# Kernel optimization log

Hardware: AMD Instinct MI355X
Metric: run time of the kernel (lower is better)

The kernel has to match this reference:

```python
import jax, jax.numpy as jnp
import numpy as np

B, ENV = 128, 512
D_IN, D1, D2 = 67, 64, 128


def _mlp(x, W1, b1, W2, b2):
    # 'deep' projection: two-layer MLP used for Q/K/V
    return jax.nn.relu(x @ W1 + b1) @ W2 + b2


def _attention(x, y, qp, kp, vp):
    # attention_mech_deep: deep Q from x, deep K/V from y, softmax over env
    Q = _mlp(x, *qp)  # (B, env, d_out)
    K = _mlp(y, *kp)
    V = _mlp(y, *vp)
    scale = 1.0 / np.sqrt(Q.shape[-1]).astype(np.float32)
    s = jnp.einsum('bid,bjd->bij', Q, K) * scale  # (B, env, env)
    return jnp.einsum('bij,bjd->bid', jax.nn.softmax(s, axis=-1), V)


def _layernorm(x, g, b, eps=1e-5):
    m = jnp.mean(x, axis=-1, keepdims=True)
    v = jnp.var(x, axis=-1, keepdims=True)
    return (x - m) * jax.lax.rsqrt(v + eps) * g + b


def _aggregate(x, W1, b1, ws, W2, b2):
    # deep_aggregator: per-node MLP + learned softmax-pooled global context
    h = jax.nn.relu(x @ W1 + b1)                      # (B, env, hid)
    alpha = jax.nn.softmax(jnp.einsum('bed,d->be', h, ws), axis=-1)
    pooled = jnp.einsum('be,bed->bd', alpha, h)[:, None, :]  # (B, 1, hid)
    return (h + pooled) @ W2 + b2                     # (B, env, out)


def setup_inputs() -> dict:
    key = jax.random.key(0)
    ks = iter(jax.random.split(key, 32))
    def p(shape, s=0.02):
        return jax.random.normal(next(ks), shape, jnp.float32) * s
    inp = {"input_graph_enc": jax.random.normal(next(ks), (B, ENV, D_IN), jnp.float32)}
    for name, di, do in [("a1", D_IN, D1), ("a2", D1, D2)]:
        for t in "qkv":
            inp[f"{name}_W{t}1"] = p((di, do))
            inp[f"{name}_b{t}1"] = jnp.zeros((do,), jnp.float32)
            inp[f"{name}_W{t}2"] = p((do, do))
            inp[f"{name}_b{t}2"] = jnp.zeros((do,), jnp.float32)
    inp["g1"] = jnp.ones((D1,), jnp.float32); inp["beta1"] = jnp.zeros((D1,), jnp.float32)
    inp["g2"] = jnp.ones((D2,), jnp.float32); inp["beta2"] = jnp.zeros((D2,), jnp.float32)
    inp["ag_W1"] = p((D2, D2)); inp["ag_b1"] = jnp.zeros((D2,), jnp.float32)
    inp["ag_ws"] = p((D2,))
    inp["ag_W2"] = p((D2, D2)); inp["ag_b2"] = jnp.zeros((D2,), jnp.float32)
    return inp


def reference(input_graph_enc,
              a1_Wq1, a1_bq1, a1_Wq2, a1_bq2,
              a1_Wk1, a1_bk1, a1_Wk2, a1_bk2,
              a1_Wv1, a1_bv1, a1_Wv2, a1_bv2,
              a2_Wq1, a2_bq1, a2_Wq2, a2_bq2,
              a2_Wk1, a2_bk1, a2_Wk2, a2_bk2,
              a2_Wv1, a2_bv1, a2_Wv2, a2_bv2,
              g1, beta1, g2, beta2,
              ag_W1, ag_b1, ag_ws, ag_W2, ag_b2):
    X = _attention(input_graph_enc, input_graph_enc,
                   (a1_Wq1, a1_bq1, a1_Wq2, a1_bq2),
                   (a1_Wk1, a1_bk1, a1_Wk2, a1_bk2),
                   (a1_Wv1, a1_bv1, a1_Wv2, a1_bv2))
    X = _layernorm(X, g1, beta1)
    X = _attention(X, X,
                   (a2_Wq1, a2_bq1, a2_Wq2, a2_bq2),
                   (a2_Wk1, a2_bk1, a2_Wk2, a2_bk2),
                   (a2_Wv1, a2_bv1, a2_Wv2, a2_bv2))
    X = _layernorm(X, g2, beta2)
    return _aggregate(X, ag_W1, ag_b1, ag_ws, ag_W2, ag_b2)  # (B, env, 128)
```

## Files before the change

### kernel.cpp

```cpp
#include <hip/hip_runtime.h>
#include <math.h>

#define ENV 512
#define NB 128

typedef __attribute__((ext_vector_type(8))) short bf16x8;
typedef __attribute__((ext_vector_type(4))) float f32x4;

__device__ inline float rsum16(float v) {
#pragma unroll
    for (int o = 8; o; o >>= 1) v += __shfl_xor(v, o, 16);
    return v;
}
__device__ inline ushort f2bf(float f) {
    unsigned u = __float_as_uint(f);
    u = u + 0x7fffu + ((u >> 16) & 1u);
    return (ushort)(u >> 16);
}
__device__ inline float bf2f(ushort h) {
    return __uint_as_float(((unsigned)h) << 16);
}

__global__ __launch_bounds__(256) void prep_kernel(
    const float* s0, const float* s1, const float* s2, const float* s3,
    const float* s4, const float* s5, const float* s6, const float* s7,
    const float* s8, const float* s9, const float* s10, const float* s11,
    const float* s12, const float* s13, ushort* wb)
{
    const float* srcs[14] = {s0,s1,s2,s3,s4,s5,s6,s7,s8,s9,s10,s11,s12,s13};
    const int Ks[14]  = {67,64,67,64,67,64, 64,128,64,128,64,128, 128,128};
    const int Cs[14]  = {64,64,64,64,64,64, 128,128,128,128,128,128, 128,128};
    const int KPs[14] = {96,64,96,64,96,64, 64,128,64,128,64,128, 128,128};
    const int offs[14]= {0,12288,20480,32768,40960,53248,
                         61440,77824,110592,126976,159744,176128,
                         208896,225280};
    const int dual[14]= {1,1,1,1,1,1,1,1,1,1,1,1,0,0};
    const int j = blockIdx.x;
    const float* src = srcs[j];
    const int K = Ks[j], C = Cs[j], KP = KPs[j], n = C * KP, d = dual[j];
    ushort* dst = wb + offs[j];
    for (int i = threadIdx.x; i < n; i += 256) {
        int c = i / KP, k = i - c * KP;
        float v = (k < K) ? src[k * C + c] : 0.f;
        ushort h = f2bf(v);
        dst[i] = h;
        if (d) dst[n + i] = f2bf(v - bf2f(h));
    }
}

__global__ __launch_bounds__(256) void xprep_kernel(
    const float* __restrict__ X, ushort* __restrict__ Xh, ushort* __restrict__ Xl)
{
    const int total = 65536 * 96;
    for (int i = blockIdx.x * 256 + threadIdx.x; i < total; i += gridDim.x * 256) {
        int r = i / 96, k = i - r * 96;
        float v = (k < 67) ? X[(long)r * 67 + k] : 0.f;
        ushort h = f2bf(v);
        Xh[i] = h;
        Xl[i] = f2bf(v - bf2f(h));
    }
}

template <int DKP, int DH, int DOUT>
__global__ __launch_bounds__(512, 1) void qk_kernel(
    const ushort* __restrict__ Xg,
    const ushort* __restrict__ Wq1, const float* __restrict__ bq1,
    const ushort* __restrict__ Wq2, const float* __restrict__ bq2,
    const ushort* __restrict__ Wk1, const float* __restrict__ bk1,
    const ushort* __restrict__ Wk2, const float* __restrict__ bk2,
    ushort* __restrict__ Qo, ushort* __restrict__ Ko)
{
    constexpr int KT1 = DKP / 32, CT1 = DH / 16, KT2 = DH / 32, CT2 = DOUT / 16;
    constexpr int W1P = DKP + 8, W2P = DH + 8, HP = DH + 8;
    __shared__ __align__(16) ushort W1s[2][DH * W1P];
    __shared__ __align__(16) ushort W2s[2][DOUT * W2P];
    __shared__ __align__(16) ushort Hs[8][16 * HP];
    const int tid = threadIdx.x, wv = tid >> 6, lid = tid & 63, g = lid >> 4, ln = lid & 15;

    for (int i = tid; i < DH * DKP / 8; i += 512) {
        int c = i / (DKP / 8), j = i - c * (DKP / 8);
        *(uint4*)&W1s[0][c * W1P + j * 8] = *(const uint4*)&Wq1[c * DKP + j * 8];
        *(uint4*)&W1s[1][c * W1P + j * 8] = *(const uint4*)&Wk1[c * DKP + j * 8];
    }
    for (int i = tid; i < DOUT * DH / 8; i += 512) {
        int c = i / (DH / 8), j = i - c * (DH / 8);
        *(uint4*)&W2s[0][c * W2P + j * 8] = *(const uint4*)&Wq2[c * DH + j * 8];
        *(uint4*)&W2s[1][c * W2P + j * 8] = *(const uint4*)&Wk2[c * DH + j * 8];
    }
    __syncthreads();

    const long row0 = (long)blockIdx.x * 128 + wv * 16;
    bf16x8 xa[KT1];
#pragma unroll
    for (int kk = 0; kk < KT1; ++kk)
        xa[kk] = *(const bf16x8*)&Xg[(row0 + ln) * DKP + kk * 32 + 8 * g];

#pragma unroll
    for (int p = 0; p < 2; ++p) {
        const ushort* w1 = W1s[p];
        const ushort* w2 = W2s[p];
        const float* b1 = p ? bk1 : bq1;
        const float* b2 = p ? bk2 : bq2;
        ushort* out = p ? Ko : Qo;
#pragma unroll
        for (int ct = 0; ct < CT1; ++ct) {
            f32x4 a = {0.f, 0.f, 0.f, 0.f};
#pragma unroll
            for (int kk = 0; kk < KT1; ++kk) {
                bf16x8 b = *(const bf16x8*)&w1[(ct * 16 + ln) * W1P + kk * 32 + 8 * g];
                a = __builtin_amdgcn_mfma_f32_16x16x32_bf16(xa[kk], b, a, 0, 0, 0);
            }
            float bb = b1[ct * 16 + ln];
#pragma unroll
            for (int i = 0; i < 4; i++)
                Hs[wv][(4 * g + i) * HP + ct * 16 + ln] = f2bf(fmaxf(a[i] + bb, 0.f));
        }
        bf16x8 ha[KT2];
#pragma unroll
        for (int kk = 0; kk < KT2; ++kk)
            ha[kk] = *(const bf16x8*)&Hs[wv][ln * HP + kk * 32 + 8 * g];
#pragma unroll
        for (int ct = 0; ct < CT2; ++ct) {
            f32x4 a = {0.f, 0.f, 0.f, 0.f};
#pragma unroll
            for (int kk = 0; kk < KT2; ++kk) {
                bf16x8 b = *(const bf16x8*)&w2[(ct * 16 + ln) * W2P + kk * 32 + 8 * g];
                a = __builtin_amdgcn_mfma_f32_16x16x32_bf16(ha[kk], b, a, 0, 0, 0);
            }
            float bb = b2[ct * 16 + ln];
            ushort* op = out + (row0 + 4 * g) * DOUT + ct * 16 + ln;
#pragma unroll
            for (int i = 0; i < 4; i++) op[(long)i * DOUT] = f2bf(a[i] + bb);
        }
    }
}

__global__ __launch_bounds__(256, 2)
void vg1_dummy() {}
template <int DKP, int DH>
__global__ __launch_bounds__(256, 2) void vg1_kernel(
    const ushort* __restrict__ Xhg, const ushort* __restrict__ Xlg,
    const ushort* __restrict__ Wv1, const float* __restrict__ bv1,
    ushort* __restrict__ Hoh, ushort* __restrict__ Hol)
{
    constexpr int KT1 = DKP / 32, CT1 = DH / 16;
    constexpr int W1P = DKP + 8, HP = DH + 8, sz1 = DH * DKP;
    constexpr int NSEG = DH / 8;
    __shared__ __align__(16) ushort W1s[2][DH * W1P];
    __shared__ __align__(16) ushort Ht[4][2][16 * HP];
    const int tid = threadIdx.x, wv = tid >> 6, lid = tid & 63, g = lid >> 4, ln = lid & 15;

    for (int i = tid; i < DH * DKP / 8; i += 256) {
        int c = i / (DKP / 8), j = i - c * (DKP / 8);
        *(uint4*)&W1s[0][c * W1P + j * 8] = *(const uint4*)&Wv1[c * DKP + j * 8];
        *(uint4*)&W1s[1][c * W1P + j * 8] = *(const uint4*)&Wv1[sz1 + c * DKP + j * 8];
    }
    __syncthreads();

    const long row0 = (long)blockIdx.x * 64 + wv * 16;
    bf16x8 xah[KT1], xal[KT1];
#pragma unroll
    for (int kk = 0; kk < KT1; ++kk) {
        xah[kk] = *(const bf16x8*)&Xhg[(row0 + ln) * DKP + kk * 32 + 8 * g];
        xal[kk] = *(const bf16x8*)&Xlg[(row0 + ln) * DKP + kk * 32 + 8 * g];
    }
#pragma unroll
    for (int ct = 0; ct < CT1; ++ct) {
        f32x4 a0 = {0.f, 0.f, 0.f, 0.f}, a1 = {0.f, 0.f, 0.f, 0.f};
#pragma unroll
        for (int kk = 0; kk < KT1; ++kk) {
            bf16x8 bh = *(const bf16x8*)&W1s[0][(ct * 16 + ln) * W1P + kk * 32 + 8 * g];
            bf16x8 bl = *(const bf16x8*)&W1s[1][(ct * 16 + ln) * W1P + kk * 32 + 8 * g];
            a0 = __builtin_amdgcn_mfma_f32_16x16x32_bf16(xah[kk], bh, a0, 0, 0, 0);
            a1 = __builtin_amdgcn_mfma_f32_16x16x32_bf16(xal[kk], bh, a1, 0, 0, 0);
            a1 = __builtin_amdgcn_mfma_f32_16x16x32_bf16(xah[kk], bl, a1, 0, 0, 0);
        }
        float bb = bv1[ct * 16 + ln];
#pragma unroll
        for (int i = 0; i < 4; i++) {
            float v = fmaxf(a0[i] + a1[i] + bb, 0.f);
            ushort h = f2bf(v);
            int idx = (4 * g + i) * HP + ct * 16 + ln;
            Ht[wv][0][idx] = h;
            Ht[wv][1][idx] = f2bf(v - bf2f(h));
        }
    }
#pragma unroll
    for (int u = 0; u < NSEG / 4; ++u) {
        int i = lid + 64 * u;
        int r = i / NSEG, sg = i - r * NSEG;
        *(uint4*)&Hoh[(row0 + r) * DH + sg * 8] = *(const uint4*)&Ht[wv][0][r * HP + sg * 8];
        *(uint4*)&Hol[(row0 + r) * DH + sg * 8] = *(const uint4*)&Ht[wv][1][r * HP + sg * 8];
    }
}

template <int DH, int DOUT>
__global__ __launch_bounds__(256, 2) void vg2_kernel(
    const ushort* __restrict__ Hoh, const ushort* __restrict__ Hol,
    const ushort* __restrict__ Wv2, const float* __restrict__ bv2,
    ushort* __restrict__ Vth, ushort* __restrict__ Vtl)
{
    constexpr int KT2 = DH / 32, CT2 = DOUT / 16;
    constexpr int W2P = DH + 8, sz2 = DOUT * DH;
    __shared__ __align__(16) ushort W2s[2][DOUT * W2P];
    const int tid = threadIdx.x, wv = tid >> 6, lid = tid & 63, g = lid >> 4, ln = lid & 15;

    for (int i = tid; i < DOUT * DH / 8; i += 256) {
        int c = i / (DH / 8), j = i - c * (DH / 8);
        *(uint4*)&W2s[0][c * W2P + j * 8] = *(const uint4*)&Wv2[c * DH + j * 8];
        *(uint4*)&W2s[1][c * W2P + j * 8] = *(const uint4*)&Wv2[sz2 + c * DH + j * 8];
    }
    __syncthreads();

    const long row0 = (long)blockIdx.x * 64 + wv * 16;
    bf16x8 vah[KT2], val[KT2];
#pragma unroll
    for (int kk = 0; kk < KT2; ++kk) {
        vah[kk] = *(const bf16x8*)&Hoh[(row0 + ln) * DH + kk * 32 + 8 * g];
        val[kk] = *(const bf16x8*)&Hol[(row0 + ln) * DH + kk * 32 + 8 * g];
    }
    const int bidx = (int)(row0 >> 9);
    const int e0 = (int)(row0 & 511) + 4 * g;
#pragma unroll
    for (int ct = 0; ct < CT2; ++ct) {
        f32x4 a0 = {0.f, 0.f, 0.f, 0.f}, a1 = {0.f, 0.f, 0.f, 0.f};
#pragma unroll
        for (int kk = 0; kk < KT2; ++kk) {
            bf16x8 bh = *(const bf16x8*)&W2s[0][(ct * 16 + ln) * W2P + kk * 32 + 8 * g];
            bf16x8 bl = *(const bf16x8*)&W2s[1][(ct * 16 + ln) * W2P + kk * 32 + 8 * g];
            a0 = __builtin_amdgcn_mfma_f32_16x16x32_bf16(vah[kk], bh, a0, 0, 0, 0);
            a1 = __builtin_amdgcn_mfma_f32_16x16x32_bf16(val[kk], bh, a1, 0, 0, 0);
            a1 = __builtin_amdgcn_mfma_f32_16x16x32_bf16(vah[kk], bl, a1, 0, 0, 0);
        }
        float bb = bv2[ct * 16 + ln];
        ushort4 hv, lv;
#pragma unroll
        for (int i = 0; i < 4; i++) {
            float v = a0[i] + a1[i] + bb;
            ushort h = f2bf(v);
            ((ushort*)&hv)[i] = h;
            ((ushort*)&lv)[i] = f2bf(v - bf2f(h));
        }
        long o = ((long)bidx * DOUT + ct * 16 + ln) * ENV + e0;
        *(ushort4*)&Vth[o] = hv;
        *(ushort4*)&Vtl[o] = lv;
    }
}

template <int D, int OMODE>
__global__ __launch_bounds__(512, 2) void attn_ln_kernel(
    const ushort* __restrict__ Qg, const ushort* __restrict__ Kg,
    const ushort* __restrict__ Vhg, const ushort* __restrict__ Vlg,
    const float* __restrict__ Gw, const float* __restrict__ Bw,
    ushort* __restrict__ Yh, ushort* __restrict__ Yl, float scale)
{
    constexpr int KT = D / 32;
    constexpr int DT = D / 16;
    constexpr int KROW = D + 8;
    constexpr int VROW = 40;
    constexpr int KSEG = D / 8;
    constexpr int KSEGS = 32 * KSEG;
    constexpr int VSEGS = D * 4;
    constexpr int TOTSEG = KSEGS + 2 * VSEGS;
    constexpr int MAXS = (TOTSEG + 511) / 512;
    constexpr int NC = ENV / 32;

    __shared__ __align__(16) ushort Ks[2][32 * KROW];
    __shared__ __align__(16) ushort Vhs[2][D * VROW];
    __shared__ __align__(16) ushort Vls[2][D * VROW];
    __shared__ __align__(16) float Ps[8][32][36];

    const int tid = threadIdx.x;
    const int wv = tid >> 6, lid = tid & 63, g = lid >> 4, ln = lid & 15;

    const int id = blockIdx.x;
    const int xcd = id & 7, rr_ = id >> 3;
    const int b = xcd + 8 * (rr_ >> 1);
    const int q0 = (rr_ & 1) * 256;

    const ushort* Kb  = Kg  + (long)b * ENV * D;
    const ushort* Vhb = Vhg + (long)b * D * ENV;
    const ushort* Vlb = Vlg + (long)b * D * ENV;

    bf16x8 qf[2][KT];
#pragma unroll
    for (int rg = 0; rg < 2; rg++) {
        const ushort* Qrow = Qg + ((long)b * ENV + q0 + wv * 32 + rg * 16 + ln) * D;
#pragma unroll
        for (int kk = 0; kk < KT; kk++)
            qf[rg][kk] = *(const bf16x8*)(Qrow + kk * 32 + 8 * g);
    }

    f32x4 acc[2][DT];
#pragma unroll
    for (int rg = 0; rg < 2; rg++)
#pragma unroll
        for (int dt = 0; dt < DT; dt++) acc[rg][dt] = (f32x4){0.f, 0.f, 0.f, 0.f};
    float lsum[2][4];
#pragma unroll
    for (int rg = 0; rg < 2; rg++)
#pragma unroll
        for (int i = 0; i < 4; i++) lsum[rg][i] = 0.f;

    uint4 stg[MAXS];
    auto LOAD = [&](int c) {
        const int k0 = c * 32;
#pragma unroll
        for (int u = 0; u < MAXS; u++) {
            int s = tid + u * 512;
            if ((TOTSEG % 512 == 0) || s < TOTSEG) {
                const ushort* src;
                if (s < KSEGS) {
                    int row = s / KSEG, sg = s % KSEG;
                    src = Kb + (long)(k0 + row) * D + sg * 8;
                } else {
                    int s2 = s - KSEGS;
                    const ushort* Vb = (s2 < VSEGS) ? Vhb : Vlb;
                    int s3 = (s2 < VSEGS) ? s2 : s2 - VSEGS;
                    int d = s3 >> 2, sg = s3 & 3;
                    src = Vb + (long)d * ENV + k0 + sg * 8;
                }
                stg[u] = *(const uint4*)src;
            }
        }
    };
    auto WRITE = [&](int buf) {
#pragma unroll
        for (int u = 0; u < MAXS; u++) {
            int s = tid + u * 512;
            if ((TOTSEG % 512 == 0) || s < TOTSEG) {
                ushort* dst;
                if (s < KSEGS) {
                    int row = s / KSEG, sg = s % KSEG;
                    dst = &Ks[buf][row * KROW + sg * 8];
                } else {
                    int s2 = s - KSEGS;
                    ushort* Vb = (s2 < VSEGS) ? &Vhs[buf][0] : &Vls[buf][0];
                    int s3 = (s2 < VSEGS) ? s2 : s2 - VSEGS;
                    int d = s3 >> 2, sg = s3 & 3;
                    dst = Vb + d * VROW + sg * 8;
                }
                *(uint4*)dst = stg[u];
            }
        }
    };

    LOAD(0);
    WRITE(0);
    __syncthreads();

    for (int c = 0; c < NC; c++) {
        const int cur = c & 1;
        if (c + 1 < NC) LOAD(c + 1);

        f32x4 sacc[2][2];
#pragma unroll
        for (int rg = 0; rg < 2; rg++)
#pragma unroll
            for (int t = 0; t < 2; t++) sacc[rg][t] = (f32x4){0.f, 0.f, 0.f, 0.f};
#pragma unroll
        for (int t = 0; t < 2; t++)
#pragma unroll
            for (int kk = 0; kk < KT; kk++) {
                bf16x8 kf = *(const bf16x8*)&Ks[cur][(16 * t + ln) * KROW + kk * 32 + 8 * g];
#pragma unroll
                for (int rg = 0; rg < 2; rg++)
                    sacc[rg][t] = __builtin_amdgcn_mfma_f32_16x16x32_bf16(qf[rg][kk], kf, sacc[rg][t], 0, 0, 0);
            }

#pragma unroll
        for (int rg = 0; rg < 2; rg++)
#pragma unroll
            for (int i = 0; i < 4; i++) {
                float p0 = __expf(fminf(sacc[rg][0][i] * scale, 50.f));
                float p1 = __expf(fminf(sacc[rg][1][i] * scale, 50.f));
                lsum[rg][i] += p0 + p1;
                Ps[wv][rg * 16 + 4 * g + i][ln]      = p0;
                Ps[wv][rg * 16 + 4 * g + i][16 + ln] = p1;
            }

        bf16x8 phi[2], plo[2];
#pragma unroll
        for (int rg = 0; rg < 2; rg++) {
            const float* pr = &Ps[wv][rg * 16 + ln][8 * g];
#pragma unroll
            for (int jj = 0; jj < 8; jj++) {
                float p = pr[jj];
                ushort h = f2bf(p);
                phi[rg][jj] = (short)h;
                plo[rg][jj] = (short)f2bf(p - bf2f(h));
            }
        }

#pragma unroll
        for (int dt = 0; dt < DT; dt++) {
            bf16x8 vh = *(const bf16x8*)&Vhs[cur][(dt * 16 + ln) * VROW + 8 * g];
            bf16x8 vl = *(const bf16x8*)&Vls[cur][(dt * 16 + ln) * VROW + 8 * g];
#pragma unroll
            for (int rg = 0; rg < 2; rg++) {
                acc[rg][dt] = __builtin_amdgcn_mfma_f32_16x16x32_bf16(phi[rg], vh, acc[rg][dt], 0, 0, 0);
                acc[rg][dt] = __builtin_amdgcn_mfma_f32_16x16x32_bf16(plo[rg], vh, acc[rg][dt], 0, 0, 0);
                acc[rg][dt] = __builtin_amdgcn_mfma_f32_16x16x32_bf16(phi[rg], vl, acc[rg][dt], 0, 0, 0);
            }
        }

        if (c + 1 < NC) WRITE(cur ^ 1);
        __syncthreads();
    }

    float gg[DT], bb[DT];
#pragma unroll
    for (int dt = 0; dt < DT; dt++) {
        gg[dt] = Gw[dt * 16 + ln];
        bb[dt] = Bw[dt * 16 + ln];
    }
#pragma unroll
    for (int rg = 0; rg < 2; rg++) {
        const long base = ((long)b * ENV + q0 + wv * 32 + rg * 16 + 4 * g) * D + ln;
#pragma unroll
        for (int i = 0; i < 4; i++) {
            float l = rsum16(lsum[rg][i]);
            float inv = 1.f / l;
            float o[DT], s1 = 0.f, s2 = 0.f;
#pragma unroll
            for (int dt = 0; dt < DT; dt++) {
                o[dt] = acc[rg][dt][i] * inv;
                s1 += o[dt];
                s2 += o[dt] * o[dt];
            }
            s1 = rsum16(s1);
            s2 = rsum16(s2);
            float mean = s1 / D;
            float var = s2 / D - mean * mean;
            float rstd = rsqrtf(var + 1e-5f);
#pragma unroll
            for (int dt = 0; dt < DT; dt++) {
                float y = (o[dt] - mean) * rstd * gg[dt] + bb[dt];
                long idx = base + (long)i * D + dt * 16;
                ushort h = f2bf(y);
                Yh[idx] = h;
                if constexpr (OMODE == 1) Yl[idx] = f2bf(y - bf2f(h));
            }
        }
    }
}

__global__ __launch_bounds__(256, 1) void agg_h_kernel(
    const ushort* __restrict__ X2b, const ushort* __restrict__ W1t,
    const float* __restrict__ b1, const float* __restrict__ wsv,
    ushort* __restrict__ H, float* __restrict__ logits)
{
    __shared__ __align__(16) ushort W1s[128 * 136];
    const int tid = threadIdx.x;
    const int wv = tid >> 6, lid = tid & 63, g = lid >> 4, ln = lid & 15;
    const long row0 = (long)blockIdx.x * 64;

    for (int i = tid; i < 128 * 16; i += 256) {
        int c = i >> 4, j = i & 15;
        *(uint4*)&W1s[c * 136 + j * 8] = *(const uint4*)&W1t[c * 128 + j * 8];
    }
    __syncthreads();

    bf16x8 ah[4];
#pragma unroll
    for (int kk = 0; kk < 4; kk++)
        ah[kk] = *(const bf16x8*)&X2b[(row0 + wv * 16 + ln) * 128 + kk * 32 + 8 * g];

    float part[4] = {0.f, 0.f, 0.f, 0.f};
#pragma unroll
    for (int ct = 0; ct < 8; ct++) {
        f32x4 a = {0.f, 0.f, 0.f, 0.f};
#pragma unroll
        for (int kk = 0; kk < 4; kk++) {
            bf16x8 bh = *(const bf16x8*)&W1s[(ct * 16 + ln) * 136 + kk * 32 + 8 * g];
            a = __builtin_amdgcn_mfma_f32_16x16x32_bf16(ah[kk], bh, a, 0, 0, 0);
        }
        float bb = b1[ct * 16 + ln], wc = wsv[ct * 16 + ln];
        ushort* hp = H + (row0 + wv * 16 + 4 * g) * 128 + ct * 16 + ln;
#pragma unroll
        for (int i = 0; i < 4; i++) {
            float v = fmaxf(a[i] + bb, 0.f);
            hp[(long)i * 128] = f2bf(v);
            part[i] += v * wc;
        }
    }
#pragma unroll
    for (int i = 0; i < 4; i++) {
        float s = rsum16(part[i]);
        if (ln == 0) logits[row0 + wv * 16 + 4 * g + i] = s;
    }
}

__global__ __launch_bounds__(256) void agg_pool_kernel(
    const ushort* __restrict__ H, const float* __restrict__ logits,
    const float* __restrict__ W2, const float* __restrict__ b2,
    float* __restrict__ bias2b)
{
    __shared__ float es[ENV];
    __shared__ float sred[4];
    __shared__ float pl[2][128];
    const int b = blockIdx.x, tid = threadIdx.x;
    const float* lg = logits + (long)b * ENV;

    float lm = -1e30f;
    for (int i = tid; i < ENV; i += 256) lm = fmaxf(lm, lg[i]);
#pragma unroll
    for (int o = 32; o; o >>= 1) lm = fmaxf(lm, __shfl_xor(lm, o, 64));
    if ((tid & 63) == 0) sred[tid >> 6] = lm;
    __syncthreads();
    float M = fmaxf(fmaxf(sred[0], sred[1]), fmaxf(sred[2], sred[3]));

    float ls = 0.f;
    for (int i = tid; i < ENV; i += 256) {
        float e = __expf(lg[i] - M);
        es[i] = e;
        ls += e;
    }
#pragma unroll
    for (int o = 32; o; o >>= 1) ls += __shfl_xor(ls, o, 64);
    __syncthreads();
    if ((tid & 63) == 0) sred[tid >> 6] = ls;
    __syncthreads();
    float S = sred[0] + sred[1] + sred[2] + sred[3];
    float inv = 1.f / S;

    int half = tid >> 7, c = tid & 127;
    float acc = 0.f;
    const ushort* Hb = H + (long)b * ENV * 128;
    for (int rr = half * 256; rr < half * 256 + 256; rr++)
        acc += es[rr] * bf2f(Hb[rr * 128 + c]);
    pl[half][c] = acc;
    __syncthreads();
    if (tid < 128) pl[0][tid] = (pl[0][tid] + pl[1][tid]) * inv;
    __syncthreads();
    if (tid < 128) {
        float a = b2[tid];
        for (int k = 0; k < 128; k++) a += pl[0][k] * W2[k * 128 + tid];
        bias2b[(long)b * 128 + tid] = a;
    }
}

__global__ __launch_bounds__(256, 1) void agg_out_kernel(
    const ushort* __restrict__ H, const ushort* __restrict__ W2t,
    const float* __restrict__ bias2b, float* __restrict__ out)
{
    __shared__ __align__(16) ushort W2s[128 * 136];
    const int tid = threadIdx.x;
    const int wv = tid >> 6, lid = tid & 63, g = lid >> 4, ln = lid & 15;
    const long row0 = (long)blockIdx.x * 64;
    const int b = (int)(row0 >> 9);

    for (int i = tid; i < 128 * 16; i += 256) {
        int c = i >> 4, j = i & 15;
        *(uint4*)&W2s[c * 136 + j * 8] = *(const uint4*)&W2t[c * 128 + j * 8];
    }
    __syncthreads();

    bf16x8 ah[4];
#pragma unroll
    for (int kk = 0; kk < 4; kk++)
        ah[kk] = *(const bf16x8*)&H[(row0 + wv * 16 + ln) * 128 + kk * 32 + 8 * g];

    const float* bb2 = bias2b + (long)b * 128;
#pragma unroll
    for (int ct = 0; ct < 8; ct++) {
        f32x4 a = {0.f, 0.f, 0.f, 0.f};
#pragma unroll
        for (int kk = 0; kk < 4; kk++) {
            bf16x8 bh = *(const bf16x8*)&W2s[(ct * 16 + ln) * 136 + kk * 32 + 8 * g];
            a = __builtin_amdgcn_mfma_f32_16x16x32_bf16(ah[kk], bh, a, 0, 0, 0);
        }
        float bb = bb2[ct * 16 + ln];
        float* op = out + (row0 + wv * 16 + 4 * g) * 128 + ct * 16 + ln;
#pragma unroll
        for (int i = 0; i < 4; i++) op[(long)i * 128] = a[i] + bb;
    }
}

extern "C" void kernel_launch(void* const* d_in, const int* in_sizes, int n_in,
                              void* d_out, int out_size, void* d_ws, size_t ws_size,
                              hipStream_t stream)
{
    const float* X = (const float*)d_in[0];
    const float* g1  = (const float*)d_in[25];
    const float* be1 = (const float*)d_in[26];
    const float* g2  = (const float*)d_in[27];
    const float* be2 = (const float*)d_in[28];

    ushort* U = (ushort*)d_ws;
    const long S1 = (long)NB * ENV * 64;
    const long S2 = (long)NB * ENV * 128;
    const long N  = (long)NB * ENV;
    const long XS = N * 96;

    ushort* XPh = U;          ushort* XPl = U + XS;
    ushort* V1h = U;          ushort* V1l = U + S1;
    ushort* K2  = U;
    ushort* Q1 = U + 2 * XS;  ushort* K1 = Q1 + S1;
    ushort* Q2 = U + 2 * XS;
    ushort* Hv1h = U + 2 * XS + S2;  ushort* Hv1l = Hv1h + S1;
    ushort* X1h  = Hv1h;             ushort* X1l  = Hv1l;
    ushort* V2h  = Hv1h;
    ushort* Hv2h = U + 2 * XS + 2 * S2;  ushort* Hv2l = Hv2h + S2;
    ushort* X2b  = Hv2h;                 ushort* Hb   = Hv2l;
    ushort* V2l = U + 2 * XS + 4 * S2;
    float*  logits = (float*)(U + 2 * XS + 5 * S2);
    float*  bias2b = logits + N;
    ushort* wb = (ushort*)(bias2b + (long)NB * 128);

    const ushort *L1q1 = wb + 0,      *L1q2 = wb + 12288,
                 *L1k1 = wb + 20480,  *L1k2 = wb + 32768,
                 *L1v1 = wb + 40960,  *L1v2 = wb + 53248,
                 *L2q1 = wb + 61440,  *L2q2 = wb + 77824,
                 *L2k1 = wb + 110592, *L2k2 = wb + 126976,
                 *L2v1 = wb + 159744, *L2v2 = wb + 176128,
                 *AW1  = wb + 208896, *AW2  = wb + 225280;

    dim3 blk(256);

    prep_kernel<<<14, blk, 0, stream>>>(
        (const float*)d_in[1], (const float*)d_in[3], (const float*)d_in[5],
        (const float*)d_in[7], (const float*)d_in[9], (const float*)d_in[11],
        (const float*)d_in[13], (const float*)d_in[15], (const float*)d_in[17],
        (const float*)d_in[19], (const float*)d_in[21], (const float*)d_in[23],
        (const float*)d_in[29], (const float*)d_in[32], wb);
    xprep_kernel<<<6144, blk, 0, stream>>>(X, XPh, XPl);

    qk_kernel<96, 64, 64><<<512, dim3(512), 0, stream>>>(
        XPh, L1q1, (const float*)d_in[2], L1q2, (const float*)d_in[4],
        L1k1, (const float*)d_in[6], L1k2, (const float*)d_in[8], Q1, K1);
    vg1_kernel<96, 64><<<1024, blk, 0, stream>>>(
        XPh, XPl, L1v1, (const float*)d_in[10], Hv1h, Hv1l);
    vg2_kernel<64, 64><<<1024, blk, 0, stream>>>(
        Hv1h, Hv1l, L1v2, (const float*)d_in[12], V1h, V1l);
    attn_ln_kernel<64, 1><<<dim3(256), dim3(512), 0, stream>>>(
        Q1, K1, V1h, V1l, g1, be1, X1h, X1l, 0.125f);

    qk_kernel<64, 128, 128><<<512, dim3(512), 0, stream>>>(
        X1h, L2q1, (const float*)d_in[14], L2q2, (const float*)d_in[16],
        L2k1, (const float*)d_in[18], L2k2, (const float*)d_in[20], Q2, K2);
    vg1_kernel<64, 128><<<1024, blk, 0, stream>>>(
        X1h, X1l, L2v1, (const float*)d_in[22], Hv2h, Hv2l);
    vg2_kernel<128, 128><<<1024, blk, 0, stream>>>(
        Hv2h, Hv2l, L2v2, (const float*)d_in[24], V2h, V2l);
    attn_ln_kernel<128, 2><<<dim3(256), dim3(512), 0, stream>>>(
        Q2, K2, V2h, V2l, g2, be2, X2b, nullptr, 0.08838834764831845f);

    agg_h_kernel<<<1024, blk, 0, stream>>>(
        X2b, AW1, (const float*)d_in[30], (const float*)d_in[31], Hb, logits);
    agg_pool_kernel<<<NB, blk, 0, stream>>>(
        Hb, logits, (const float*)d_in[32], (const float*)d_in[33], bias2b);
    agg_out_kernel<<<1024, blk, 0, stream>>>(
        Hb, AW2, bias2b, (float*)d_out);
}
```

Before: 372.3 us.

## Compute transposed scores to keep softmax probabilities in registers, dropping LDS staging

Swaps the MFMA operand order so the score tile comes out transposed: each lane holds the 8 key-column values it needs as the A operand of the P·V MFMA. This removes the per-chunk write/read of probabilities through the Ps shared buffer and its per-row sum bookkeeping. V fragments are now gathered as two 4-element pieces to match the new key ordering, and row sums are reduced with cross-group shuffles at the end. The smaller LDS footprint lets the launch-bounds occupancy hint rise from 2 to 4 blocks per CU, which may increase register pressure.

```diff
diff --git a/kernel.cpp b/kernel.cpp
--- a/kernel.cpp
+++ b/kernel.cpp
@@ -135,8 +135,6 @@
     }
 }
 
-__global__ __launch_bounds__(256, 2)
-void vg1_dummy() {}
 template <int DKP, int DH>
 __global__ __launch_bounds__(256, 2) void vg1_kernel(
     const ushort* __restrict__ Xhg, const ushort* __restrict__ Xlg,
@@ -248,7 +246,7 @@
 }
 
 template <int D, int OMODE>
-__global__ __launch_bounds__(512, 2) void attn_ln_kernel(
+__global__ __launch_bounds__(512, 4) void attn_ln_kernel(
     const ushort* __restrict__ Qg, const ushort* __restrict__ Kg,
     const ushort* __restrict__ Vhg, const ushort* __restrict__ Vlg,
     const float* __restrict__ Gw, const float* __restrict__ Bw,
@@ -268,7 +266,6 @@
     __shared__ __align__(16) ushort Ks[2][32 * KROW];
     __shared__ __align__(16) ushort Vhs[2][D * VROW];
     __shared__ __align__(16) ushort Vls[2][D * VROW];
-    __shared__ __align__(16) float Ps[8][32][36];
 
     const int tid = threadIdx.x;
     const int wv = tid >> 6, lid = tid & 63, g = lid >> 4, ln = lid & 15;
@@ -296,11 +293,7 @@
     for (int rg = 0; rg < 2; rg++)
 #pragma unroll
         for (int dt = 0; dt < DT; dt++) acc[rg][dt] = (f32x4){0.f, 0.f, 0.f, 0.f};
-    float lsum[2][4];
-#pragma unroll
-    for (int rg = 0; rg < 2; rg++)
-#pragma unroll
-        for (int i = 0; i < 4; i++) lsum[rg][i] = 0.f;
+    float lsum[2] = {0.f, 0.f};
 
     uint4 stg[MAXS];
     auto LOAD = [&](int c) {
@@ -365,37 +358,38 @@
                 bf16x8 kf = *(const bf16x8*)&Ks[cur][(16 * t + ln) * KROW + kk * 32 + 8 * g];
 #pragma unroll
                 for (int rg = 0; rg < 2; rg++)
-                    sacc[rg][t] = __builtin_amdgcn_mfma_f32_16x16x32_bf16(qf[rg][kk], kf, sacc[rg][t], 0, 0, 0);
-            }
-
-#pragma unroll
-        for (int rg = 0; rg < 2; rg++)
-#pragma unroll
-            for (int i = 0; i < 4; i++) {
-                float p0 = __expf(fminf(sacc[rg][0][i] * scale, 50.f));
-                float p1 = __expf(fminf(sacc[rg][1][i] * scale, 50.f));
-                lsum[rg][i] += p0 + p1;
-                Ps[wv][rg * 16 + 4 * g + i][ln]      = p0;
-                Ps[wv][rg * 16 + 4 * g + i][16 + ln] = p1;
+                    sacc[rg][t] = __builtin_amdgcn_mfma_f32_16x16x32_bf16(kf, qf[rg][kk], sacc[rg][t], 0, 0, 0);
             }
 
         bf16x8 phi[2], plo[2];
 #pragma unroll
         for (int rg = 0; rg < 2; rg++) {
-            const float* pr = &Ps[wv][rg * 16 + ln][8 * g];
-#pragma unroll
-            for (int jj = 0; jj < 8; jj++) {
-                float p = pr[jj];
+            float ls = 0.f;
+#pragma unroll
+            for (int j = 0; j < 8; j++) {
+                float s = (j < 4) ? sacc[rg][0][j] : sacc[rg][1][j - 4];
+                float p = __expf(fminf(s * scale, 50.f));
+                ls += p;
                 ushort h = f2bf(p);
-                phi[rg][jj] = (short)h;
-                plo[rg][jj] = (short)f2bf(p - bf2f(h));
-            }
+                phi[rg][j] = (short)h;
+                plo[rg][j] = (short)f2bf(p - bf2f(h));
+            }
+            lsum[rg] += ls;
         }
 
 #pragma unroll
         for (int dt = 0; dt < DT; dt++) {
-            bf16x8 vh = *(const bf16x8*)&Vhs[cur][(dt * 16 + ln) * VROW + 8 * g];
-            bf16x8 vl = *(const bf16x8*)&Vls[cur][(dt * 16 + ln) * VROW + 8 * g];
+            const ushort* vrh = &Vhs[cur][(dt * 16 + ln) * VROW];
+            const ushort* vrl = &Vls[cur][(dt * 16 + ln) * VROW];
+            ushort4 ha = *(const ushort4*)(vrh + 4 * g);
+            ushort4 hb = *(const ushort4*)(vrh + 16 + 4 * g);
+            ushort4 la = *(const ushort4*)(vrl + 4 * g);
+            ushort4 lb = *(const ushort4*)(vrl + 16 + 4 * g);
+            bf16x8 vh, vl;
+            vh[0] = (short)ha.x; vh[1] = (short)ha.y; vh[2] = (short)ha.z; vh[3] = (short)ha.w;
+            vh[4] = (short)hb.x; vh[5] = (short)hb.y; vh[6] = (short)hb.z; vh[7] = (short)hb.w;
+            vl[0] = (short)la.x; vl[1] = (short)la.y; vl[2] = (short)la.z; vl[3] = (short)la.w;
+            vl[4] = (short)lb.x; vl[5] = (short)lb.y; vl[6] = (short)lb.z; vl[7] = (short)lb.w;
 #pragma unroll
             for (int rg = 0; rg < 2; rg++) {
                 acc[rg][dt] = __builtin_amdgcn_mfma_f32_16x16x32_bf16(phi[rg], vh, acc[rg][dt], 0, 0, 0);
@@ -408,6 +402,15 @@
         __syncthreads();
     }
 
+    float lr[2];
+#pragma unroll
+    for (int rg = 0; rg < 2; rg++) {
+        float v = lsum[rg];
+        v += __shfl_xor(v, 16);
+        v += __shfl_xor(v, 32);
+        lr[rg] = v;
+    }
+
     float gg[DT], bb[DT];
 #pragma unroll
     for (int dt = 0; dt < DT; dt++) {
@@ -419,7 +422,7 @@
         const long base = ((long)b * ENV + q0 + wv * 32 + rg * 16 + 4 * g) * D + ln;
 #pragma unroll
         for (int i = 0; i < 4; i++) {
-            float l = rsum16(lsum[rg][i]);
+            float l = __shfl(lr[rg], 4 * g + i, 16);
             float inv = 1.f / l;
             float o[DT], s1 = 0.f, s2 = 0.f;
 #pragma unroll
```

Result: slower. 489.2 us (+31.4%).
